# Kernel tuning notes

Hardware: AMD Instinct MI355X
Metric: run time of the kernel (lower is better)

Reference implementation:

```python
import jax, jax.numpy as jnp
import numpy as np

QMAX = 127.0
EPS = 1e-12


def _smooth_quant(x, col_scale):
    """Per-row int8 quantization of (x * col_scale).
    Returns (q, row_scale): q holds integer values in [-127, 127] (kept in f32,
    exactly representable), row_scale is abs-max/127 per row."""
    xs = x * col_scale                                  # [R, K]
    row_scale = jnp.max(jnp.abs(xs), axis=-1) / QMAX    # [R]
    row_scale = jnp.maximum(row_scale, EPS)
    q = jnp.clip(jnp.round(xs / row_scale[:, None]), -QMAX, QMAX)
    return q, row_scale


def setup_inputs() -> dict:
    key = jax.random.key(0)
    k1, k2, k3 = jax.random.split(key, 3)
    B, S, K, N = 4, 8192, 1024, 1024
    input_ = jax.random.normal(k1, (B, S, K), dtype=jnp.float32)
    weight = jax.random.normal(k2, (N, K), dtype=jnp.float32) * 0.02
    bias = jax.random.normal(k3, (N,), dtype=jnp.float32) * 0.01
    return {"input": input_, "weight": weight, "bias": bias}


def reference(input, weight, bias):
    x2 = input.reshape(-1, input.shape[-1])             # [M, K]
    # SmoothQuant smoothing scale: sqrt(colmax(|x|) * colmax(|w|)), shape [K]
    in_max = jnp.max(jnp.abs(x2), axis=0)
    w_max = jnp.max(jnp.abs(weight), axis=0)
    smooth_scale = jnp.sqrt(jnp.maximum(in_max * w_max, EPS))
    # quantize activations divided by smooth_scale, weights multiplied by it
    x_q, x_s = _smooth_quant(x2, 1.0 / smooth_scale)    # [M,K], [M]
    w_q, w_s = _smooth_quant(weight, smooth_scale)      # [N,K], [N]
    # int8 matmul (emulated exactly in f32) + row/col dequant scales + bias
    acc = x_q @ w_q.T                                   # [M, N]
    out = acc * x_s[:, None] * w_s[None, :] + bias
    return out.reshape(*input.shape[:-1], weight.shape[0])
```

## Files before the change

### kernel.cpp

```cpp
#include <hip/hip_runtime.h>


typedef int v4i __attribute__((ext_vector_type(4)));

__device__ __forceinline__ void gld_lds16(const void* g, void* l) {
    __builtin_amdgcn_global_load_lds(
        (const __attribute__((address_space(1))) void*)g,
        (__attribute__((address_space(3))) void*)l,
        16, 0, 0);
}

__global__ __launch_bounds__(256) void colmax_part_kernel(const float* __restrict__ src,
                                                          int rows, int rpb, int K,
                                                          float* __restrict__ partial) {
    const int c = threadIdx.x * 4;
    int r0 = blockIdx.x * rpb;
    int r1 = r0 + rpb; if (r1 > rows) r1 = rows;
    float m0 = 0.f, m1 = 0.f, m2 = 0.f, m3 = 0.f;
    const float* p = src + (size_t)r0 * K + c;
#pragma unroll 8
    for (int r = r0; r < r1; ++r, p += K) {
        float4 v = *(const float4*)p;
        m0 = fmaxf(m0, fabsf(v.x));
        m1 = fmaxf(m1, fabsf(v.y));
        m2 = fmaxf(m2, fabsf(v.z));
        m3 = fmaxf(m3, fabsf(v.w));
    }
    float4 o; o.x = m0; o.y = m1; o.z = m2; o.w = m3;
    *(float4*)(partial + (size_t)blockIdx.x * K + c) = o;
}

__global__ void finalize_kernel(const float* __restrict__ px, int nx,
                                const float* __restrict__ pw, int nw,
                                float* __restrict__ smooth, float* __restrict__ inv_s, int K) {
    int c = blockIdx.x * blockDim.x + threadIdx.x;
    if (c >= K) return;
    float mx = 0.f, mw = 0.f;
    for (int r = 0; r < nx; ++r) mx = fmaxf(mx, px[(size_t)r * K + c]);
    for (int r = 0; r < nw; ++r) mw = fmaxf(mw, pw[(size_t)r * K + c]);
    float s = sqrtf(fmaxf(mx * mw, 1e-12f));
    smooth[c] = s;
    inv_s[c]  = 1.0f / s;
}

__global__ __launch_bounds__(256) void quant_rows_wave_kernel(
    const float* __restrict__ src, const float* __restrict__ colscale,
    signed char* __restrict__ q, float* __restrict__ rowscale, int K) {
    const int wave = threadIdx.x >> 6, lane = threadIdx.x & 63;
    const int row = blockIdx.x * 4 + wave;
    const float* srow = src + (size_t)row * K + lane * 16;
    const float* crow = colscale + lane * 16;
    float xs[16];
    float mv = 0.f;
#pragma unroll
    for (int i = 0; i < 4; ++i) {
        float4 v  = *(const float4*)(srow + i * 4);
        float4 cs = *(const float4*)(crow + i * 4);
        xs[i*4+0] = v.x * cs.x; xs[i*4+1] = v.y * cs.y;
        xs[i*4+2] = v.z * cs.z; xs[i*4+3] = v.w * cs.w;
        mv = fmaxf(mv, fmaxf(fmaxf(fabsf(xs[i*4+0]), fabsf(xs[i*4+1])),
                             fmaxf(fabsf(xs[i*4+2]), fabsf(xs[i*4+3]))));
    }
#pragma unroll
    for (int off = 32; off > 0; off >>= 1)
        mv = fmaxf(mv, __shfl_xor(mv, off, 64));
    const float rs = fmaxf(mv / 127.0f, 1e-12f);
    unsigned pk[4];
#pragma unroll
    for (int i = 0; i < 4; ++i) {
        float q0 = fminf(fmaxf(rintf(xs[i*4+0] / rs), -127.f), 127.f);
        float q1 = fminf(fmaxf(rintf(xs[i*4+1] / rs), -127.f), 127.f);
        float q2 = fminf(fmaxf(rintf(xs[i*4+2] / rs), -127.f), 127.f);
        float q3 = fminf(fmaxf(rintf(xs[i*4+3] / rs), -127.f), 127.f);
        int b0 = (int)q0, b1 = (int)q1, b2 = (int)q2, b3 = (int)q3;
        pk[i] = (unsigned)(b0 & 0xff) | ((unsigned)(b1 & 0xff) << 8)
              | ((unsigned)(b2 & 0xff) << 16) | ((unsigned)(b3 & 0xff) << 24);
    }
    *(uint4*)(q + (size_t)row * K + lane * 16) = make_uint4(pk[0], pk[1], pk[2], pk[3]);
    if (lane == 0) rowscale[row] = rs;
}

__global__ __launch_bounds__(256) void gemm_i8_kernel(
    const signed char* __restrict__ Aq,
    const signed char* __restrict__ Bq,
    const float* __restrict__ xs,
    const float* __restrict__ wsc,
    const float* __restrict__ bias,
    float* __restrict__ out,
    int M, int N, int K) {
    __shared__ __align__(16) signed char As[2][128 * 64];
    __shared__ __align__(16) signed char Bs[2][128 * 64];

    const int tid  = threadIdx.x;
    const int lane = tid & 63;
    const int wave = tid >> 6;
    const int waveM = (wave >> 1) * 64;
    const int waveN = (wave & 1) * 64;

    const int bid = blockIdx.x;
    const int bm = ((bid & 7) * 32 + (bid >> 6)) * 128;
    const int bn = ((bid >> 3) & 7) * 128;

    const int srow  = tid >> 2;
    const int qslot = tid & 3;
    const int gq    = (qslot ^ ((srow >> 1) & 3)) * 16;
    const int ldsOff = srow * 64 + qslot * 16;

    const signed char* aG0 = Aq + (size_t)(bm + srow) * K + gq;
    const signed char* aG1 = Aq + (size_t)(bm + 64 + srow) * K + gq;
    const signed char* bG0 = Bq + (size_t)(bn + srow) * K + gq;
    const signed char* bG1 = Bq + (size_t)(bn + 64 + srow) * K + gq;

    v4i acc[4][4] = {};

    const int fr = lane & 15;
    const int fp = ((lane >> 4) ^ ((fr >> 1) & 3)) * 16;

#define STAGE(k0, b)                                   \
    do {                                               \
        gld_lds16(aG0 + (k0), &As[b][ldsOff]);         \
        gld_lds16(aG1 + (k0), &As[b][ldsOff + 4096]);  \
        gld_lds16(bG0 + (k0), &Bs[b][ldsOff]);         \
        gld_lds16(bG1 + (k0), &Bs[b][ldsOff + 4096]);  \
    } while (0)

#define COMPUTE(b)                                                        \
    do {                                                                  \
        v4i af[4], bf[4];                                                 \
        _Pragma("unroll")                                                 \
        for (int i = 0; i < 4; ++i)                                       \
            af[i] = *(const v4i*)&As[b][(waveM + i * 16 + fr) * 64 + fp]; \
        _Pragma("unroll")                                                 \
        for (int j = 0; j < 4; ++j)                                       \
            bf[j] = *(const v4i*)&Bs[b][(waveN + j * 16 + fr) * 64 + fp]; \
        _Pragma("unroll")                                                 \
        for (int i = 0; i < 4; ++i)                                       \
            _Pragma("unroll")                                             \
            for (int j = 0; j < 4; ++j)                                   \
                acc[i][j] = __builtin_amdgcn_mfma_i32_16x16x64_i8(        \
                    af[i], bf[j], acc[i][j], 0, 0, 0);                    \
    } while (0)

    STAGE(0, 0);
    for (int k0 = 0; k0 < K; k0 += 128) {
        __syncthreads();
        if (k0 + 64 < K) STAGE(k0 + 64, 1);
        COMPUTE(0);
        __syncthreads();
        if (k0 + 128 < K) STAGE(k0 + 128, 0);
        COMPUTE(1);
    }
#undef STAGE
#undef COMPUTE

    const int orow0 = bm + waveM + (lane >> 4) * 4;
    const int ocol0 = bn + waveN + fr;
#pragma unroll
    for (int j = 0; j < 4; ++j) {
        const int col = ocol0 + j * 16;
        const float wn = wsc[col];
        const float bv = bias[col];
#pragma unroll
        for (int i = 0; i < 4; ++i) {
            const int rbase = orow0 + i * 16;
#pragma unroll
            for (int r = 0; r < 4; ++r) {
                const int row = rbase + r;
                float v = (float)acc[i][j][r] * xs[row];
                out[(size_t)row * N + col] = v * wn + bv;
            }
        }
    }
}

extern "C" void kernel_launch(void* const* d_in, const int* in_sizes, int n_in,
                              void* d_out, int out_size, void* d_ws, size_t ws_size,
                              hipStream_t stream) {
    const float* x    = (const float*)d_in[0];
    const float* w    = (const float*)d_in[1];
    const float* bias = (const float*)d_in[2];
    float* out = (float*)d_out;

    const int N = in_sizes[2];
    const int K = in_sizes[1] / N;
    const int M = in_sizes[0] / K;

    char* ws = (char*)d_ws;
    float* p1x       = (float*)(ws);
    float* p2x       = (float*)(ws + 4194304);
    float* pw        = (float*)(ws + 4259840);
    float* smooth    = (float*)(ws + 4325376);
    float* inv_s     = (float*)(ws + 4329472);
    float* w_s       = (float*)(ws + 4333568);
    float* x_s       = (float*)(ws + 4337664);
    signed char* x_q = (signed char*)(ws + 4468736);
    signed char* w_q = x_q + (size_t)M * K;

    colmax_part_kernel<<<1024, 256, 0, stream>>>(x, M, 32, K, p1x);
    colmax_part_kernel<<<16, 256, 0, stream>>>(p1x, 1024, 64, K, p2x);
    colmax_part_kernel<<<16, 256, 0, stream>>>(w, N, 64, K, pw);
    finalize_kernel<<<(K + 255) / 256, 256, 0, stream>>>(p2x, 16, pw, 16, smooth, inv_s, K);
    quant_rows_wave_kernel<<<N / 4, 256, 0, stream>>>(w, smooth, w_q, w_s, K);
    quant_rows_wave_kernel<<<M / 4, 256, 0, stream>>>(x, inv_s, x_q, x_s, K);
    gemm_i8_kernel<<<(M / 128) * (N / 128), 256, 0, stream>>>(x_q, w_q, x_s, w_s, bias, out, M, N, K);
}
```

Measured before the change: 335.7 us.

## Rewrite int8 GEMM with 256x256 tiles, 8 waves, and phased LDS pipeline

The int8 GEMM moves from 128x128 tiles with 4 waves to 256x256 tiles with 8 waves, each wave computing a 128x64 sub-tile. K is handled in 128-wide steps, double-buffered across 128 KB of LDS. Loads are issued in four interleaved phases, with explicit vmcnt waits, barriers and setprio around each MFMA burst, so global-to-LDS copies overlap compute. This should raise arithmetic intensity and cut load stalls, at the cost of heavy LDS use that limits occupancy, and it assumes M and N divide by 256 and K by 128.

```diff
diff --git a/kernel.cpp b/kernel.cpp
--- a/kernel.cpp
+++ b/kernel.cpp
@@ -80,7 +80,7 @@
     if (lane == 0) rowscale[row] = rs;
 }
 
-__global__ __launch_bounds__(256) void gemm_i8_kernel(
+__global__ __launch_bounds__(512, 2) void gemm_i8_kernel(
     const signed char* __restrict__ Aq,
     const signed char* __restrict__ Bq,
     const float* __restrict__ xs,
@@ -88,87 +88,130 @@
     const float* __restrict__ bias,
     float* __restrict__ out,
     int M, int N, int K) {
-    __shared__ __align__(16) signed char As[2][128 * 64];
-    __shared__ __align__(16) signed char Bs[2][128 * 64];
+    __shared__ __align__(16) signed char As[65536];
+    __shared__ __align__(16) signed char Bs[65536];
 
     const int tid  = threadIdx.x;
     const int lane = tid & 63;
     const int wave = tid >> 6;
-    const int waveM = (wave >> 1) * 64;
-    const int waveN = (wave & 1) * 64;
-
-    const int bid = blockIdx.x;
-    const int bm = ((bid & 7) * 32 + (bid >> 6)) * 128;
-    const int bn = ((bid >> 3) & 7) * 128;
-
-    const int srow  = tid >> 2;
-    const int qslot = tid & 3;
-    const int gq    = (qslot ^ ((srow >> 1) & 3)) * 16;
-    const int ldsOff = srow * 64 + qslot * 16;
-
-    const signed char* aG0 = Aq + (size_t)(bm + srow) * K + gq;
-    const signed char* aG1 = Aq + (size_t)(bm + 64 + srow) * K + gq;
-    const signed char* bG0 = Bq + (size_t)(bn + srow) * K + gq;
-    const signed char* bG1 = Bq + (size_t)(bn + 64 + srow) * K + gq;
-
-    v4i acc[4][4] = {};
-
+    const int wm = wave >> 2;
+    const int wn = wave & 3;
+    const int g  = lane >> 4;
     const int fr = lane & 15;
-    const int fp = ((lane >> 4) ^ ((fr >> 1) & 3)) * 16;
-
-#define STAGE(k0, b)                                   \
-    do {                                               \
-        gld_lds16(aG0 + (k0), &As[b][ldsOff]);         \
-        gld_lds16(aG1 + (k0), &As[b][ldsOff + 4096]);  \
-        gld_lds16(bG0 + (k0), &Bs[b][ldsOff]);         \
-        gld_lds16(bG1 + (k0), &Bs[b][ldsOff + 4096]);  \
+
+    const int NT = K >> 7;
+
+    const int nwg = gridDim.x;
+    const int wg  = (blockIdx.x & 7) * (nwg >> 3) + (blockIdx.x >> 3);
+    const int nTn = N >> 8;
+    const int tm = wg / nTn, tn = wg % nTn;
+    const int bm = tm << 8, bn = tn << 8;
+
+    const int srow = tid >> 2;
+    const int schk = (tid & 3) ^ (srow & 3);
+    const signed char* srcA0 = Aq + (size_t)(bm + srow) * K + schk * 16;
+    const signed char* srcA1 = srcA0 + (size_t)128 * K;
+    const signed char* srcB0 = Bq + (size_t)(bn + srow) * K + schk * 16;
+    const signed char* srcB1 = srcB0 + (size_t)128 * K;
+    const int ldsSt = tid * 16;
+
+    const int swz   = (g ^ (fr & 3)) * 16;
+    const int aBase = (wm * 128 + fr) * 64 + swz;
+    const int bBase = (wn * 64 + fr) * 64 + swz;
+
+    v4i acc[8][4] = {};
+    v4i bf[4];
+
+#define STAGE_A(T, KS) do { \
+        const int go_ = (T) * 128 + (KS) * 64; \
+        signed char* l_ = &As[((T) & 1) * 32768 + (KS) * 16384 + ldsSt]; \
+        gld_lds16(srcA0 + go_, l_); \
+        gld_lds16(srcA1 + go_, l_ + 8192); \
     } while (0)
-
-#define COMPUTE(b)                                                        \
-    do {                                                                  \
-        v4i af[4], bf[4];                                                 \
-        _Pragma("unroll")                                                 \
-        for (int i = 0; i < 4; ++i)                                       \
-            af[i] = *(const v4i*)&As[b][(waveM + i * 16 + fr) * 64 + fp]; \
-        _Pragma("unroll")                                                 \
-        for (int j = 0; j < 4; ++j)                                       \
-            bf[j] = *(const v4i*)&Bs[b][(waveN + j * 16 + fr) * 64 + fp]; \
-        _Pragma("unroll")                                                 \
-        for (int i = 0; i < 4; ++i)                                       \
-            _Pragma("unroll")                                             \
-            for (int j = 0; j < 4; ++j)                                   \
-                acc[i][j] = __builtin_amdgcn_mfma_i32_16x16x64_i8(        \
-                    af[i], bf[j], acc[i][j], 0, 0, 0);                    \
+#define STAGE_B(T, KS) do { \
+        const int go_ = (T) * 128 + (KS) * 64; \
+        signed char* l_ = &Bs[((T) & 1) * 32768 + (KS) * 16384 + ldsSt]; \
+        gld_lds16(srcB0 + go_, l_); \
+        gld_lds16(srcB1 + go_, l_ + 8192); \
     } while (0)
 
-    STAGE(0, 0);
-    for (int k0 = 0; k0 < K; k0 += 128) {
-        __syncthreads();
-        if (k0 + 64 < K) STAGE(k0 + 64, 1);
-        COMPUTE(0);
-        __syncthreads();
-        if (k0 + 128 < K) STAGE(k0 + 128, 0);
-        COMPUTE(1);
-    }
-#undef STAGE
-#undef COMPUTE
-
-    const int orow0 = bm + waveM + (lane >> 4) * 4;
-    const int ocol0 = bn + waveN + fr;
+#define PHASE(BUF, KS, MH, STG, WAIT) \
+    do { \
+        const int hb_ = (BUF) * 32768 + (KS) * 16384; \
+        v4i af[4]; \
+        _Pragma("unroll") \
+        for (int i = 0; i < 4; ++i) \
+            af[i] = *(const v4i*)&As[hb_ + aBase + ((MH) * 4 + i) * 1024]; \
+        if ((MH) == 0) { \
+            _Pragma("unroll") \
+            for (int j = 0; j < 4; ++j) \
+                bf[j] = *(const v4i*)&Bs[hb_ + bBase + j * 1024]; \
+        } \
+        STG; \
+        asm volatile("s_waitcnt " WAIT ::: "memory"); \
+        asm volatile("s_barrier" ::: "memory"); \
+        asm volatile("s_waitcnt lgkmcnt(0)" ::: "memory"); \
+        __builtin_amdgcn_sched_barrier(0); \
+        __builtin_amdgcn_s_setprio(1); \
+        _Pragma("unroll") \
+        for (int i = 0; i < 4; ++i) \
+            _Pragma("unroll") \
+            for (int j = 0; j < 4; ++j) \
+                acc[(MH) * 4 + i][j] = __builtin_amdgcn_mfma_i32_16x16x64_i8( \
+                    af[i], bf[j], acc[(MH) * 4 + i][j], 0, 0, 0); \
+        __builtin_amdgcn_s_setprio(0); \
+        asm volatile("s_barrier" ::: "memory"); \
+    } while (0)
+
+    STAGE_A(0, 0); STAGE_B(0, 0);
+    STAGE_A(0, 1); STAGE_B(0, 1);
+    STAGE_A(1, 0); STAGE_B(1, 0);
+    asm volatile("s_waitcnt vmcnt(4)" ::: "memory");
+    asm volatile("s_barrier" ::: "memory");
+
+    for (int t = 0; t < NT - 2; ++t) {
+        const int buf = t & 1;
+        PHASE(buf, 0, 0, STAGE_A(t + 1, 1), "vmcnt(8)");
+        PHASE(buf, 0, 1, STAGE_B(t + 1, 1), "vmcnt(8)");
+        PHASE(buf, 1, 0, STAGE_A(t + 2, 0), "vmcnt(8)");
+        PHASE(buf, 1, 1, STAGE_B(t + 2, 0), "vmcnt(8)");
+    }
+    {
+        const int t = NT - 2, buf = t & 1;
+        PHASE(buf, 0, 0, STAGE_A(t + 1, 1), "vmcnt(8)");
+        PHASE(buf, 0, 1, STAGE_B(t + 1, 1), "vmcnt(8)");
+        PHASE(buf, 1, 0, (void)0, "vmcnt(8)");
+        PHASE(buf, 1, 1, (void)0, "vmcnt(4)");
+    }
+    {
+        const int buf = (NT - 1) & 1;
+        PHASE(buf, 0, 0, (void)0, "vmcnt(4)");
+        PHASE(buf, 0, 1, (void)0, "vmcnt(0)");
+        PHASE(buf, 1, 0, (void)0, "vmcnt(0)");
+        PHASE(buf, 1, 1, (void)0, "vmcnt(0)");
+    }
+#undef PHASE
+#undef STAGE_A
+#undef STAGE_B
+
+    const int orow0 = bm + wm * 128 + g * 4;
+    const int ocol0 = bn + wn * 64 + fr;
+    float wv[4], bvv[4];
 #pragma unroll
     for (int j = 0; j < 4; ++j) {
-        const int col = ocol0 + j * 16;
-        const float wn = wsc[col];
-        const float bv = bias[col];
-#pragma unroll
-        for (int i = 0; i < 4; ++i) {
-            const int rbase = orow0 + i * 16;
-#pragma unroll
-            for (int r = 0; r < 4; ++r) {
-                const int row = rbase + r;
-                float v = (float)acc[i][j][r] * xs[row];
-                out[(size_t)row * N + col] = v * wn + bv;
-            }
+        wv[j]  = wsc[ocol0 + j * 16];
+        bvv[j] = bias[ocol0 + j * 16];
+    }
+#pragma unroll
+    for (int i = 0; i < 8; ++i) {
+#pragma unroll
+        for (int r = 0; r < 4; ++r) {
+            const int row = orow0 + i * 16 + r;
+            const float xv = xs[row];
+            float* op = out + (size_t)row * N + ocol0;
+#pragma unroll
+            for (int j = 0; j < 4; ++j)
+                op[j * 16] = (float)acc[i][j][r] * xv * wv[j] + bvv[j];
         }
     }
 }
@@ -202,5 +245,5 @@
     finalize_kernel<<<(K + 255) / 256, 256, 0, stream>>>(p2x, 16, pw, 16, smooth, inv_s, K);
     quant_rows_wave_kernel<<<N / 4, 256, 0, stream>>>(w, smooth, w_q, w_s, K);
     quant_rows_wave_kernel<<<M / 4, 256, 0, stream>>>(x, inv_s, x_q, x_s, K);
-    gemm_i8_kernel<<<(M / 128) * (N / 128), 256, 0, stream>>>(x_q, w_q, x_s, w_s, bias, out, M, N, K);
-}
+    gemm_i8_kernel<<<(M / 256) * (N / 256), 512, 0, stream>>>(x_q, w_q, x_s, w_s, bias, out, M, N, K);
+}
```

Result: faster. 317.5 us (-5.4%).
